# Optimization experiments

Measured on AMD Instinct MI355X. Metric: run time of the kernel, lower is better.

Reference implementation:

```python
import jax, jax.numpy as jnp
import numpy as np

B, S, F, H = 128, 1024, 512, 128


def setup_inputs() -> dict:
    key = jax.random.key(0)
    ks = jax.random.split(key, 12)
    # ragged valid lengths; force one full-length sequence so padded max == S
    lengths = jax.random.randint(ks[0], (B,), S // 4, S + 1)
    lengths = lengths.at[0].set(S)
    mask = (jnp.arange(S)[None, :] < lengths[:, None]).astype(jnp.float32)
    x = jax.random.normal(ks[1], (B, S, F), jnp.float32) * mask[:, :, None]
    s = 1.0 / np.sqrt(H)

    def u(k, shape):
        return jax.random.uniform(k, shape, jnp.float32, -s, s)

    return {
        "x": x,
        "Wp": u(ks[2], (H, F)), "bp": u(ks[3], (H,)),
        "Wih0": u(ks[4], (3 * H, H)), "Whh0": u(ks[5], (3 * H, H)),
        "bih0": u(ks[6], (3 * H,)), "bhh0": u(ks[7], (3 * H,)),
        "Wih1": u(ks[8], (3 * H, H)), "Whh1": u(ks[9], (3 * H, H)),
        "bih1": u(ks[10], (3 * H,)), "bhh1": u(ks[11], (3 * H,)),
    }


def _gru_layer(xs, Wih, Whh, bih, bhh):
    # xs: [S, B, H_in] -> outputs [S, B, H]; torch nn.GRU gate math (r,z,n order)
    xg = jnp.einsum('sbi,gi->sbg', xs, Wih) + bih  # precompute input gates [S,B,3H]
    Hh = Whh.shape[1]

    def step(h, xg_t):
        hg = h @ Whh.T + bhh
        xr, xz, xn = jnp.split(xg_t, 3, axis=-1)
        hr, hz, hn = jnp.split(hg, 3, axis=-1)
        r = jax.nn.sigmoid(xr + hr)
        z = jax.nn.sigmoid(xz + hz)
        n = jnp.tanh(xn + r * hn)
        h_new = (1.0 - z) * n + z * h
        return h_new, h_new

    h0 = jnp.zeros((xs.shape[1], Hh), xs.dtype)
    _, hs = jax.lax.scan(step, h0, xg)
    return hs


def reference(x, Wp, bp, Wih0, Whh0, bih0, bhh0, Wih1, Whh1, bih1, bhh1):
    # valid lengths: rows whose feature-sum is nonzero
    lengths = (jnp.sum(x, axis=-1) != 0).astype(jnp.int32).sum(axis=1)  # [B]
    proj = x @ Wp.T + bp  # [B,S,H]
    # sort by descending length (module returns outputs in SORTED order, no unsort)
    order = jnp.argsort(-lengths)
    sorted_lengths = lengths[order]
    xs = jnp.transpose(proj[order], (1, 0, 2))  # [S,B,H]
    h1 = _gru_layer(xs, Wih0, Whh0, bih0, bhh0)
    h2 = _gru_layer(h1, Wih1, Whh1, bih1, bhh1)
    out = jnp.transpose(h2, (1, 0, 2))  # [B,S,H]
    # pad_packed_sequence zeros outputs beyond each valid length
    valid = (jnp.arange(S)[None, :] < sorted_lengths[:, None]).astype(out.dtype)
    out = out * valid[:, :, None]
    # mean over padded length (max length == S here), zeros included, as in torch
    return out.mean(axis=1)
```

## Files before the change

kernel.cpp:

```cpp
#include <hip/hip_runtime.h>
#include <hip/hip_bf16.h>

#define BB 128
#define SS 1024
#define FF 512
#define HH 128
#define G3 384

typedef __attribute__((ext_vector_type(8))) short bf16x8;
typedef __attribute__((ext_vector_type(4))) float f32x4;
typedef _Float16 half2_t __attribute__((ext_vector_type(2)));

__global__ void zero_len_kernel(int* len) { len[threadIdx.x] = 0; }

__global__ void lengths_kernel(const float* __restrict__ x, int* __restrict__ len) {
    int wave = threadIdx.x >> 6;
    int lane = threadIdx.x & 63;
    long row = (long)blockIdx.x * 4 + wave;
    const float4* p = (const float4*)&x[row * FF + lane * 8];
    float4 v0 = p[0], v1 = p[1];
    float s = v0.x + v0.y + v0.z + v0.w + v1.x + v1.y + v1.z + v1.w;
    #pragma unroll
    for (int off = 32; off > 0; off >>= 1) s += __shfl_down(s, off, 64);
    if (lane == 0 && s != 0.0f) atomicAdd(&len[row >> 10], 1);
}

__global__ void rank_kernel(const int* __restrict__ len, int* __restrict__ rank) {
    int i = threadIdx.x;
    int li = len[i];
    int r = 0;
    for (int jj = 0; jj < BB; jj++) {
        int lj = len[jj];
        if (lj > li || (lj == li && jj < i)) r++;
    }
    rank[i] = r;
}

__device__ __forceinline__ short bf_hi(float w, float& hf) {
    unsigned u = __builtin_bit_cast(unsigned, w);
    unsigned r = (u + 0x7FFFu + ((u >> 16) & 1u)) & 0xFFFF0000u;
    hf = __builtin_bit_cast(float, r);
    return (short)(r >> 16);
}
__device__ __forceinline__ short bf_rn(float w) {
    unsigned u = __builtin_bit_cast(unsigned, w);
    unsigned r = u + 0x7FFFu + ((u >> 16) & 1u);
    return (short)(r >> 16);
}

__global__ __launch_bounds__(256) void gemm_mfma(
    const float* __restrict__ A, const float* __restrict__ W,
    const float* __restrict__ bias, float* __restrict__ C,
    int M, int N, int K)
{
    const int tid  = threadIdx.x;
    const int wvid = tid >> 6;
    const int lane = tid & 63;
    const int m0   = blockIdx.x * 64 + wvid * 16;
    const int n0   = blockIdx.y * 128;
    const int KS   = K >> 5;

    __shared__ __align__(16) short sh[2][8][64][8];

    f32x4 acc[8];
    #pragma unroll
    for (int i = 0; i < 8; i++) acc[i] = (f32x4){0.f, 0.f, 0.f, 0.f};

    const int arow = m0 + (lane & 15);
    const int koff = (lane >> 4) << 3;

    for (int ks = 0; ks < KS; ks++) {
        __syncthreads();
        #pragma unroll
        for (int i = 0; i < 2; i++) {
            int p  = tid + i * 256;
            int nt = p >> 6, ln = p & 63;
            const float* src = &W[(size_t)(n0 + nt * 16 + (ln & 15)) * K
                                  + ks * 32 + ((ln >> 4) << 3)];
            float w8[8];
            *(float4*)&w8[0] = *(const float4*)&src[0];
            *(float4*)&w8[4] = *(const float4*)&src[4];
            short hi8[8], lo8[8];
            #pragma unroll
            for (int e = 0; e < 8; e++) {
                float hf; hi8[e] = bf_hi(w8[e], hf);
                lo8[e] = bf_rn(w8[e] - hf);
            }
            *(bf16x8*)&sh[0][nt][ln][0] = *(bf16x8*)hi8;
            *(bf16x8*)&sh[1][nt][ln][0] = *(bf16x8*)lo8;
        }
        const float* ap = &A[(size_t)arow * K + ks * 32 + koff];
        float av[8];
        *(float4*)&av[0] = *(const float4*)&ap[0];
        *(float4*)&av[4] = *(const float4*)&ap[4];
        short ah[8], al[8];
        #pragma unroll
        for (int e = 0; e < 8; e++) {
            float hf; ah[e] = bf_hi(av[e], hf);
            al[e] = bf_rn(av[e] - hf);
        }
        bf16x8 ahi = *(bf16x8*)ah, alo = *(bf16x8*)al;
        __syncthreads();
        #pragma unroll
        for (int nt = 0; nt < 8; nt++) {
            bf16x8 bhi = *(bf16x8*)&sh[0][nt][lane][0];
            bf16x8 blo = *(bf16x8*)&sh[1][nt][lane][0];
            acc[nt] = __builtin_amdgcn_mfma_f32_16x16x32_bf16(ahi, bhi, acc[nt], 0, 0, 0);
            acc[nt] = __builtin_amdgcn_mfma_f32_16x16x32_bf16(ahi, blo, acc[nt], 0, 0, 0);
            acc[nt] = __builtin_amdgcn_mfma_f32_16x16x32_bf16(alo, bhi, acc[nt], 0, 0, 0);
        }
    }
    const int crow = m0 + ((lane >> 4) << 2);
    const int ccol = n0 + (lane & 15);
    #pragma unroll
    for (int nt = 0; nt < 8; nt++) {
        int col = ccol + nt * 16;
        float bv = bias[col];
        #pragma unroll
        for (int r = 0; r < 4; r++)
            C[(size_t)(crow + r) * N + col] = acc[nt][r] + bv;
    }
}

__device__ __forceinline__ float fast_sigmoid(float x) {
    return __builtin_amdgcn_rcpf(1.0f + __expf(-x));
}
__device__ __forceinline__ float fast_tanh(float x) {
    return 1.0f - 2.0f * __builtin_amdgcn_rcpf(1.0f + __expf(2.0f * x));
}
__device__ __forceinline__ half2_t bc16(unsigned u) {
    return __builtin_bit_cast(half2_t, u);
}
__device__ __forceinline__ unsigned pk16(float x, float y) {
    half2_t h; h[0] = (_Float16)x; h[1] = (_Float16)y;
    return __builtin_bit_cast(unsigned, h);
}
__device__ __forceinline__ float fdot2_(half2_t a, half2_t b, float c) {
#if __has_builtin(__builtin_amdgcn_fdot2)
    return __builtin_amdgcn_fdot2(a, b, c, false);
#else
    return c + (float)a[0] * (float)b[0] + (float)a[1] * (float)b[1];
#endif
}

template<int FINAL>
__global__ __launch_bounds__(1024, 4) void gru_rec(
    const float* __restrict__ xg,
    const float* __restrict__ Whh,
    const float* __restrict__ bhh,
    float* __restrict__ h_out,
    const int* __restrict__ len,
    const int* __restrict__ rank)
{
    const int b   = blockIdx.x;
    const int tid = threadIdx.x;
    const int j   = tid >> 3;
    const int k8  = tid & 7;

    __shared__ __align__(16) _Float16 h16[2][HH];
    __shared__ __align__(16) float    h32[2][HH];

    unsigned wv[24];
    #pragma unroll
    for (int g = 0; g < 3; g++) {
        const float* wr = &Whh[(size_t)(g * HH + j) * HH + k8 * 16];
        #pragma unroll
        for (int m = 0; m < 8; m++) wv[g * 8 + m] = pk16(wr[2 * m], wr[2 * m + 1]);
    }

    float b_r = 0.f, b_z = 0.f, b_n = 0.f;
    if (k8 == 0) { b_r = bhh[j]; b_z = bhh[HH + j]; b_n = bhh[2 * HH + j]; }
    const float* xgb = xg + (size_t)b * SS * G3;

    if (tid < HH) { h16[0][tid] = (_Float16)0.f; h32[0][tid] = 0.f; }
    float hprev = 0.0f, osum = 0.0f;
    const int L = FINAL ? len[b] : 0;

    float xr = 0.f, xz = 0.f, xn = 0.f;
    if (k8 == 0) { xr = xgb[j]; xz = xgb[HH + j]; xn = xgb[2 * HH + j]; }
    __syncthreads();

    for (int t = 0; t < SS; t++) {
        #pragma unroll
        for (int m = 0; m < 24; m += 4)
            asm volatile("" : "+v"(wv[m]), "+v"(wv[m + 1]),
                              "+v"(wv[m + 2]), "+v"(wv[m + 3]));

        if (!FINAL && t > 0 && tid >= 64 && tid < 96) {
            int c = tid - 64;
            float4 hv = ((const float4*)h32[t & 1])[c];
            *(float4*)&h_out[((size_t)b * SS + (t - 1)) * HH + c * 4] = hv;
        }
        float nxr = 0.f, nxz = 0.f, nxn = 0.f;
        if (k8 == 0 && t + 1 < SS) {
            const float* p = xgb + (size_t)(t + 1) * G3;
            nxr = p[j]; nxz = p[HH + j]; nxn = p[2 * HH + j];
        }
        const unsigned* hp = (const unsigned*)(&h16[t & 1][0]) + k8 * 8;
        uint4 hv0 = *(const uint4*)hp;
        uint4 hv1 = *(const uint4*)(hp + 4);
        half2_t q0 = bc16(hv0.x), q1 = bc16(hv0.y), q2 = bc16(hv0.z), q3 = bc16(hv0.w);
        half2_t q4 = bc16(hv1.x), q5 = bc16(hv1.y), q6 = bc16(hv1.z), q7 = bc16(hv1.w);

        float a0, a1, a2, c0, c1, c2;
        a0 = fdot2_(bc16(wv[0]),  q0, 0.f); c0 = fdot2_(bc16(wv[1]),  q1, 0.f);
        a0 = fdot2_(bc16(wv[2]),  q2, a0);  c0 = fdot2_(bc16(wv[3]),  q3, c0);
        a0 = fdot2_(bc16(wv[4]),  q4, a0);  c0 = fdot2_(bc16(wv[5]),  q5, c0);
        a0 = fdot2_(bc16(wv[6]),  q6, a0);  c0 = fdot2_(bc16(wv[7]),  q7, c0);
        a1 = fdot2_(bc16(wv[8]),  q0, 0.f); c1 = fdot2_(bc16(wv[9]),  q1, 0.f);
        a1 = fdot2_(bc16(wv[10]), q2, a1);  c1 = fdot2_(bc16(wv[11]), q3, c1);
        a1 = fdot2_(bc16(wv[12]), q4, a1);  c1 = fdot2_(bc16(wv[13]), q5, c1);
        a1 = fdot2_(bc16(wv[14]), q6, a1);  c1 = fdot2_(bc16(wv[15]), q7, c1);
        a2 = fdot2_(bc16(wv[16]), q0, 0.f); c2 = fdot2_(bc16(wv[17]), q1, 0.f);
        a2 = fdot2_(bc16(wv[18]), q2, a2);  c2 = fdot2_(bc16(wv[19]), q3, c2);
        a2 = fdot2_(bc16(wv[20]), q4, a2);  c2 = fdot2_(bc16(wv[21]), q5, c2);
        a2 = fdot2_(bc16(wv[22]), q6, a2);  c2 = fdot2_(bc16(wv[23]), q7, c2);

        float s0 = a0 + c0, s1 = a1 + c1, s2 = a2 + c2;
        s0 += __shfl_xor(s0, 1, 64); s1 += __shfl_xor(s1, 1, 64); s2 += __shfl_xor(s2, 1, 64);
        s0 += __shfl_xor(s0, 2, 64); s1 += __shfl_xor(s1, 2, 64); s2 += __shfl_xor(s2, 2, 64);
        s0 += __shfl_xor(s0, 4, 64); s1 += __shfl_xor(s1, 4, 64); s2 += __shfl_xor(s2, 4, 64);

        if (k8 == 0) {
            float r = fast_sigmoid(xr + s0 + b_r);
            float z = fast_sigmoid(xz + s1 + b_z);
            float n = fast_tanh(xn + r * (s2 + b_n));
            float h = (1.0f - z) * n + z * hprev;
            hprev = h;
            h16[(t + 1) & 1][j] = (_Float16)h;
            h32[(t + 1) & 1][j] = h;
            if (FINAL) { if (t < L) osum += h; }
        }
        xr = nxr; xz = nxz; xn = nxn;
        __syncthreads();
    }
    if (!FINAL && tid >= 64 && tid < 96) {
        int c = tid - 64;
        float4 hv = ((const float4*)h32[SS & 1])[c];
        *(float4*)&h_out[((size_t)b * SS + (SS - 1)) * HH + c * 4] = hv;
    }
    if (FINAL && k8 == 0) {
        h_out[(size_t)rank[b] * HH + j] = osum * (1.0f / (float)SS);
    }
}

extern "C" void kernel_launch(void* const* d_in, const int* in_sizes, int n_in,
                              void* d_out, int out_size, void* d_ws, size_t ws_size,
                              hipStream_t stream) {
    const float* x    = (const float*)d_in[0];
    const float* Wp   = (const float*)d_in[1];
    const float* bp   = (const float*)d_in[2];
    const float* Wih0 = (const float*)d_in[3];
    const float* Whh0 = (const float*)d_in[4];
    const float* bih0 = (const float*)d_in[5];
    const float* bhh0 = (const float*)d_in[6];
    const float* Wih1 = (const float*)d_in[7];
    const float* Whh1 = (const float*)d_in[8];
    const float* bih1 = (const float*)d_in[9];
    const float* bhh1 = (const float*)d_in[10];
    float* out = (float*)d_out;

    int* len  = (int*)d_ws;
    int* rank = len + 128;
    float* proj = (float*)((char*)d_ws + 4096);
    float* xgb  = proj + (size_t)BB * SS * HH;

    zero_len_kernel<<<1, 128, 0, stream>>>(len);
    lengths_kernel<<<(BB * SS) / 4, 256, 0, stream>>>(x, len);
    rank_kernel<<<1, 128, 0, stream>>>(len, rank);

    gemm_mfma<<<dim3(BB * SS / 64, 1), 256, 0, stream>>>(x, Wp, bp, proj,
                                                         BB * SS, HH, FF);
    gemm_mfma<<<dim3(BB * SS / 64, 3), 256, 0, stream>>>(proj, Wih0, bih0, xgb,
                                                         BB * SS, G3, HH);
    gru_rec<0><<<BB, 1024, 0, stream>>>(xgb, Whh0, bhh0, proj, len, rank);

    gemm_mfma<<<dim3(BB * SS / 64, 3), 256, 0, stream>>>(proj, Wih1, bih1, xgb,
                                                         BB * SS, G3, HH);
    gru_rec<1><<<BB, 1024, 0, stream>>>(xgb, Whh1, bhh1, out, len, rank);
}
```

Baseline: 2.451 ms.

## Stage packed fp16 Whh in LDS and halve GRU recurrence block size

A new pre-pass packs each recurrent weight matrix into an fp16 layout suited to how it is read. The GRU recurrence kernel copies that packed matrix into shared memory (96 KB) and runs with 512 threads instead of 1024, so each thread handles a quarter of a row instead of an eighth. This trades register-resident weights for LDS reads each step and saves one shuffle-reduction stage and half the wavefronts in the per-step barrier. The risk is added LDS bandwidth and latency on the serial critical path, plus the large shared allocation limiting occupancy.

```diff
diff --git a/kernel.cpp b/kernel.cpp
--- a/kernel.cpp
+++ b/kernel.cpp
@@ -143,10 +143,22 @@
 #endif
 }
 
+__global__ void pack_whh(const float* __restrict__ Whh, uint4* __restrict__ wp) {
+    int tid = threadIdx.x, r = blockIdx.x;
+    int g = r >> 2, i = r & 3, j = tid >> 2, kq = tid & 3;
+    const float* src = &Whh[(size_t)(g * HH + j) * HH + kq * 32 + i * 8];
+    uint4 o;
+    o.x = pk16(src[0], src[1]);
+    o.y = pk16(src[2], src[3]);
+    o.z = pk16(src[4], src[5]);
+    o.w = pk16(src[6], src[7]);
+    wp[r * 512 + tid] = o;
+}
+
 template<int FINAL>
-__global__ __launch_bounds__(1024, 4) void gru_rec(
+__global__ __launch_bounds__(512) void gru_rec(
+    const uint4* __restrict__ wp,
     const float* __restrict__ xg,
-    const float* __restrict__ Whh,
     const float* __restrict__ bhh,
     float* __restrict__ h_out,
     const int* __restrict__ len,
@@ -154,22 +166,18 @@
 {
     const int b   = blockIdx.x;
     const int tid = threadIdx.x;
-    const int j   = tid >> 3;
-    const int k8  = tid & 7;
-
+    const int j   = tid >> 2;
+    const int kq  = tid & 3;
+
+    __shared__ __align__(16) uint4    wlds[12 * 512];
     __shared__ __align__(16) _Float16 h16[2][HH];
     __shared__ __align__(16) float    h32[2][HH];
 
-    unsigned wv[24];
     #pragma unroll
-    for (int g = 0; g < 3; g++) {
-        const float* wr = &Whh[(size_t)(g * HH + j) * HH + k8 * 16];
-        #pragma unroll
-        for (int m = 0; m < 8; m++) wv[g * 8 + m] = pk16(wr[2 * m], wr[2 * m + 1]);
-    }
+    for (int r = 0; r < 12; r++) wlds[r * 512 + tid] = wp[r * 512 + tid];
 
     float b_r = 0.f, b_z = 0.f, b_n = 0.f;
-    if (k8 == 0) { b_r = bhh[j]; b_z = bhh[HH + j]; b_n = bhh[2 * HH + j]; }
+    if (kq == 0) { b_r = bhh[j]; b_z = bhh[HH + j]; b_n = bhh[2 * HH + j]; }
     const float* xgb = xg + (size_t)b * SS * G3;
 
     if (tid < HH) { h16[0][tid] = (_Float16)0.f; h32[0][tid] = 0.f; }
@@ -177,14 +185,14 @@
     const int L = FINAL ? len[b] : 0;
 
     float xr = 0.f, xz = 0.f, xn = 0.f;
-    if (k8 == 0) { xr = xgb[j]; xz = xgb[HH + j]; xn = xgb[2 * HH + j]; }
+    if (kq == 0) { xr = xgb[j]; xz = xgb[HH + j]; xn = xgb[2 * HH + j]; }
     __syncthreads();
 
     for (int t = 0; t < SS; t++) {
-        #pragma unroll
-        for (int m = 0; m < 24; m += 4)
-            asm volatile("" : "+v"(wv[m]), "+v"(wv[m + 1]),
-                              "+v"(wv[m + 2]), "+v"(wv[m + 3]));
+        int base = 0;
+        asm volatile("" : "+v"(base));
+        const uint4* wlA = wlds + tid + base;
+        const uint4* wlB = wlds + 8 * 512 + tid + base;
 
         if (!FINAL && t > 0 && tid >= 64 && tid < 96) {
             int c = tid - 64;
@@ -192,36 +200,58 @@
             *(float4*)&h_out[((size_t)b * SS + (t - 1)) * HH + c * 4] = hv;
         }
         float nxr = 0.f, nxz = 0.f, nxn = 0.f;
-        if (k8 == 0 && t + 1 < SS) {
+        if (kq == 0 && t + 1 < SS) {
             const float* p = xgb + (size_t)(t + 1) * G3;
             nxr = p[j]; nxz = p[HH + j]; nxn = p[2 * HH + j];
         }
-        const unsigned* hp = (const unsigned*)(&h16[t & 1][0]) + k8 * 8;
-        uint4 hv0 = *(const uint4*)hp;
-        uint4 hv1 = *(const uint4*)(hp + 4);
-        half2_t q0 = bc16(hv0.x), q1 = bc16(hv0.y), q2 = bc16(hv0.z), q3 = bc16(hv0.w);
-        half2_t q4 = bc16(hv1.x), q5 = bc16(hv1.y), q6 = bc16(hv1.z), q7 = bc16(hv1.w);
-
-        float a0, a1, a2, c0, c1, c2;
-        a0 = fdot2_(bc16(wv[0]),  q0, 0.f); c0 = fdot2_(bc16(wv[1]),  q1, 0.f);
-        a0 = fdot2_(bc16(wv[2]),  q2, a0);  c0 = fdot2_(bc16(wv[3]),  q3, c0);
-        a0 = fdot2_(bc16(wv[4]),  q4, a0);  c0 = fdot2_(bc16(wv[5]),  q5, c0);
-        a0 = fdot2_(bc16(wv[6]),  q6, a0);  c0 = fdot2_(bc16(wv[7]),  q7, c0);
-        a1 = fdot2_(bc16(wv[8]),  q0, 0.f); c1 = fdot2_(bc16(wv[9]),  q1, 0.f);
-        a1 = fdot2_(bc16(wv[10]), q2, a1);  c1 = fdot2_(bc16(wv[11]), q3, c1);
-        a1 = fdot2_(bc16(wv[12]), q4, a1);  c1 = fdot2_(bc16(wv[13]), q5, c1);
-        a1 = fdot2_(bc16(wv[14]), q6, a1);  c1 = fdot2_(bc16(wv[15]), q7, c1);
-        a2 = fdot2_(bc16(wv[16]), q0, 0.f); c2 = fdot2_(bc16(wv[17]), q1, 0.f);
-        a2 = fdot2_(bc16(wv[18]), q2, a2);  c2 = fdot2_(bc16(wv[19]), q3, c2);
-        a2 = fdot2_(bc16(wv[20]), q4, a2);  c2 = fdot2_(bc16(wv[21]), q5, c2);
-        a2 = fdot2_(bc16(wv[22]), q6, a2);  c2 = fdot2_(bc16(wv[23]), q7, c2);
-
-        float s0 = a0 + c0, s1 = a1 + c1, s2 = a2 + c2;
+        const uint4* hp = (const uint4*)(&h16[t & 1][0]) + kq * 4;
+        uint4 hq0 = hp[0], hq1 = hp[1], hq2 = hp[2], hq3 = hp[3];
+
+        float s0, s1, s2;
+        {
+            uint4 w0 = wlA[0 * 512], w1 = wlA[1 * 512], w2 = wlA[2 * 512], w3 = wlA[3 * 512];
+            float aA = fdot2_(bc16(w0.x), bc16(hq0.x), 0.f);
+            float aB = fdot2_(bc16(w0.y), bc16(hq0.y), 0.f);
+            aA = fdot2_(bc16(w0.z), bc16(hq0.z), aA); aB = fdot2_(bc16(w0.w), bc16(hq0.w), aB);
+            aA = fdot2_(bc16(w1.x), bc16(hq1.x), aA); aB = fdot2_(bc16(w1.y), bc16(hq1.y), aB);
+            aA = fdot2_(bc16(w1.z), bc16(hq1.z), aA); aB = fdot2_(bc16(w1.w), bc16(hq1.w), aB);
+            aA = fdot2_(bc16(w2.x), bc16(hq2.x), aA); aB = fdot2_(bc16(w2.y), bc16(hq2.y), aB);
+            aA = fdot2_(bc16(w2.z), bc16(hq2.z), aA); aB = fdot2_(bc16(w2.w), bc16(hq2.w), aB);
+            aA = fdot2_(bc16(w3.x), bc16(hq3.x), aA); aB = fdot2_(bc16(w3.y), bc16(hq3.y), aB);
+            aA = fdot2_(bc16(w3.z), bc16(hq3.z), aA); aB = fdot2_(bc16(w3.w), bc16(hq3.w), aB);
+            s0 = aA + aB;
+        }
+        {
+            uint4 w0 = wlA[4 * 512], w1 = wlA[5 * 512], w2 = wlA[6 * 512], w3 = wlA[7 * 512];
+            float aA = fdot2_(bc16(w0.x), bc16(hq0.x), 0.f);
+            float aB = fdot2_(bc16(w0.y), bc16(hq0.y), 0.f);
+            aA = fdot2_(bc16(w0.z), bc16(hq0.z), aA); aB = fdot2_(bc16(w0.w), bc16(hq0.w), aB);
+            aA = fdot2_(bc16(w1.x), bc16(hq1.x), aA); aB = fdot2_(bc16(w1.y), bc16(hq1.y), aB);
+            aA = fdot2_(bc16(w1.z), bc16(hq1.z), aA); aB = fdot2_(bc16(w1.w), bc16(hq1.w), aB);
+            aA = fdot2_(bc16(w2.x), bc16(hq2.x), aA); aB = fdot2_(bc16(w2.y), bc16(hq2.y), aB);
+            aA = fdot2_(bc16(w2.z), bc16(hq2.z), aA); aB = fdot2_(bc16(w2.w), bc16(hq2.w), aB);
+            aA = fdot2_(bc16(w3.x), bc16(hq3.x), aA); aB = fdot2_(bc16(w3.y), bc16(hq3.y), aB);
+            aA = fdot2_(bc16(w3.z), bc16(hq3.z), aA); aB = fdot2_(bc16(w3.w), bc16(hq3.w), aB);
+            s1 = aA + aB;
+        }
+        {
+            uint4 w0 = wlB[0 * 512], w1 = wlB[1 * 512], w2 = wlB[2 * 512], w3 = wlB[3 * 512];
+            float aA = fdot2_(bc16(w0.x), bc16(hq0.x), 0.f);
+            float aB = fdot2_(bc16(w0.y), bc16(hq0.y), 0.f);
+            aA = fdot2_(bc16(w0.z), bc16(hq0.z), aA); aB = fdot2_(bc16(w0.w), bc16(hq0.w), aB);
+            aA = fdot2_(bc16(w1.x), bc16(hq1.x), aA); aB = fdot2_(bc16(w1.y), bc16(hq1.y), aB);
+            aA = fdot2_(bc16(w1.z), bc16(hq1.z), aA); aB = fdot2_(bc16(w1.w), bc16(hq1.w), aB);
+            aA = fdot2_(bc16(w2.x), bc16(hq2.x), aA); aB = fdot2_(bc16(w2.y), bc16(hq2.y), aB);
+            aA = fdot2_(bc16(w2.z), bc16(hq2.z), aA); aB = fdot2_(bc16(w2.w), bc16(hq2.w), aB);
+            aA = fdot2_(bc16(w3.x), bc16(hq3.x), aA); aB = fdot2_(bc16(w3.y), bc16(hq3.y), aB);
+            aA = fdot2_(bc16(w3.z), bc16(hq3.z), aA); aB = fdot2_(bc16(w3.w), bc16(hq3.w), aB);
+            s2 = aA + aB;
+        }
+
         s0 += __shfl_xor(s0, 1, 64); s1 += __shfl_xor(s1, 1, 64); s2 += __shfl_xor(s2, 1, 64);
         s0 += __shfl_xor(s0, 2, 64); s1 += __shfl_xor(s1, 2, 64); s2 += __shfl_xor(s2, 2, 64);
-        s0 += __shfl_xor(s0, 4, 64); s1 += __shfl_xor(s1, 4, 64); s2 += __shfl_xor(s2, 4, 64);
-
-        if (k8 == 0) {
+
+        if (kq == 0) {
             float r = fast_sigmoid(xr + s0 + b_r);
             float z = fast_sigmoid(xz + s1 + b_z);
             float n = fast_tanh(xn + r * (s2 + b_n));
@@ -239,7 +269,7 @@
         float4 hv = ((const float4*)h32[SS & 1])[c];
         *(float4*)&h_out[((size_t)b * SS + (SS - 1)) * HH + c * 4] = hv;
     }
-    if (FINAL && k8 == 0) {
+    if (FINAL && kq == 0) {
         h_out[(size_t)rank[b] * HH + j] = osum * (1.0f / (float)SS);
     }
 }
@@ -262,20 +292,24 @@
 
     int* len  = (int*)d_ws;
     int* rank = len + 128;
-    float* proj = (float*)((char*)d_ws + 4096);
+    uint4* wp0 = (uint4*)((char*)d_ws + 4096);
+    uint4* wp1 = wp0 + 12 * 512;
+    float* proj = (float*)((char*)d_ws + 4096 + 2 * 12 * 512 * 16 + 4096);
     float* xgb  = proj + (size_t)BB * SS * HH;
 
     zero_len_kernel<<<1, 128, 0, stream>>>(len);
     lengths_kernel<<<(BB * SS) / 4, 256, 0, stream>>>(x, len);
     rank_kernel<<<1, 128, 0, stream>>>(len, rank);
+    pack_whh<<<12, 512, 0, stream>>>(Whh0, wp0);
+    pack_whh<<<12, 512, 0, stream>>>(Whh1, wp1);
 
     gemm_mfma<<<dim3(BB * SS / 64, 1), 256, 0, stream>>>(x, Wp, bp, proj,
                                                          BB * SS, HH, FF);
     gemm_mfma<<<dim3(BB * SS / 64, 3), 256, 0, stream>>>(proj, Wih0, bih0, xgb,
                                                          BB * SS, G3, HH);
-    gru_rec<0><<<BB, 1024, 0, stream>>>(xgb, Whh0, bhh0, proj, len, rank);
+    gru_rec<0><<<BB, 512, 0, stream>>>(wp0, xgb, bhh0, proj, len, rank);
 
     gemm_mfma<<<dim3(BB * SS / 64, 3), 256, 0, stream>>>(proj, Wih1, bih1, xgb,
                                                          BB * SS, G3, HH);
-    gru_rec<1><<<BB, 1024, 0, stream>>>(xgb, Whh1, bhh1, out, len, rank);
-}
+    gru_rec<1><<<BB, 512, 0, stream>>>(wp1, xgb, bhh1, out, len, rank);
+}
```

Result: faster. 2.162 ms (-11.8%).

## Shrink GRU recurrence to 256-thread blocks with Whh held in AGPRs

Applied to the files above, without the earlier changes.

The recurrent kernel drops from 1024 to 256 threads per block. Each thread now computes two hidden units over a 32-wide slice of K, and the 96 packed fp16 weight words per thread sit in accumulation registers (AGPRs), read back each step with v_accvgpr_read. The aim is a cheaper per-step __syncthreads, a shorter shuffle reduction (2 levels instead of 3), and vectorized float2 gate loads and stores. In exchange each thread does about four times more serial dot-product work per step, plus an AGPR read per weight word, which lengthens the per-timestep critical path.

```diff
diff --git a/kernel.cpp b/kernel.cpp
--- a/kernel.cpp
+++ b/kernel.cpp
@@ -143,8 +143,13 @@
 #endif
 }
 
+#define AW(N) asm volatile("v_accvgpr_write_b32 a" #N ", %0" :: "v"(wt[(N) & 15]) : "a" #N)
+#define DOT(N, ACC) do { unsigned _w; \
+    asm volatile("v_accvgpr_read_b32 %0, a" #N : "=v"(_w)); \
+    ACC = fdot2_(bc16(_w), bc16(hw[(N) & 15]), ACC); } while (0)
+
 template<int FINAL>
-__global__ __launch_bounds__(1024, 4) void gru_rec(
+__global__ __launch_bounds__(256, 1) void gru_rec(
     const float* __restrict__ xg,
     const float* __restrict__ Whh,
     const float* __restrict__ bhh,
@@ -154,84 +159,142 @@
 {
     const int b   = blockIdx.x;
     const int tid = threadIdx.x;
-    const int j   = tid >> 3;
-    const int k8  = tid & 7;
-
-    __shared__ __align__(16) _Float16 h16[2][HH];
+    const int j2  = tid >> 2;
+    const int kq  = tid & 3;
+    const int j0  = 2 * j2, j1 = 2 * j2 + 1;
+
+    __shared__ __align__(16) unsigned h16u[2][64];
     __shared__ __align__(16) float    h32[2][HH];
 
-    unsigned wv[24];
-    #pragma unroll
-    for (int g = 0; g < 3; g++) {
-        const float* wr = &Whh[(size_t)(g * HH + j) * HH + k8 * 16];
-        #pragma unroll
-        for (int m = 0; m < 8; m++) wv[g * 8 + m] = pk16(wr[2 * m], wr[2 * m + 1]);
-    }
-
-    float b_r = 0.f, b_z = 0.f, b_n = 0.f;
-    if (k8 == 0) { b_r = bhh[j]; b_z = bhh[HH + j]; b_n = bhh[2 * HH + j]; }
+    unsigned wt[16];
+    { const float* wr = &Whh[(size_t)(0 * HH + j0) * HH + kq * 32];
+      #pragma unroll
+      for (int m = 0; m < 16; m++) wt[m] = pk16(wr[2*m], wr[2*m+1]); }
+    AW(0);  AW(1);  AW(2);  AW(3);  AW(4);  AW(5);  AW(6);  AW(7);
+    AW(8);  AW(9);  AW(10); AW(11); AW(12); AW(13); AW(14); AW(15);
+    { const float* wr = &Whh[(size_t)(1 * HH + j0) * HH + kq * 32];
+      #pragma unroll
+      for (int m = 0; m < 16; m++) wt[m] = pk16(wr[2*m], wr[2*m+1]); }
+    AW(16); AW(17); AW(18); AW(19); AW(20); AW(21); AW(22); AW(23);
+    AW(24); AW(25); AW(26); AW(27); AW(28); AW(29); AW(30); AW(31);
+    { const float* wr = &Whh[(size_t)(2 * HH + j0) * HH + kq * 32];
+      #pragma unroll
+      for (int m = 0; m < 16; m++) wt[m] = pk16(wr[2*m], wr[2*m+1]); }
+    AW(32); AW(33); AW(34); AW(35); AW(36); AW(37); AW(38); AW(39);
+    AW(40); AW(41); AW(42); AW(43); AW(44); AW(45); AW(46); AW(47);
+    { const float* wr = &Whh[(size_t)(0 * HH + j1) * HH + kq * 32];
+      #pragma unroll
+      for (int m = 0; m < 16; m++) wt[m] = pk16(wr[2*m], wr[2*m+1]); }
+    AW(48); AW(49); AW(50); AW(51); AW(52); AW(53); AW(54); AW(55);
+    AW(56); AW(57); AW(58); AW(59); AW(60); AW(61); AW(62); AW(63);
+    { const float* wr = &Whh[(size_t)(1 * HH + j1) * HH + kq * 32];
+      #pragma unroll
+      for (int m = 0; m < 16; m++) wt[m] = pk16(wr[2*m], wr[2*m+1]); }
+    AW(64); AW(65); AW(66); AW(67); AW(68); AW(69); AW(70); AW(71);
+    AW(72); AW(73); AW(74); AW(75); AW(76); AW(77); AW(78); AW(79);
+    { const float* wr = &Whh[(size_t)(2 * HH + j1) * HH + kq * 32];
+      #pragma unroll
+      for (int m = 0; m < 16; m++) wt[m] = pk16(wr[2*m], wr[2*m+1]); }
+    AW(80); AW(81); AW(82); AW(83); AW(84); AW(85); AW(86); AW(87);
+    AW(88); AW(89); AW(90); AW(91); AW(92); AW(93); AW(94); AW(95);
+
+    float2 brv = {0.f, 0.f}, bzv = {0.f, 0.f}, bnv = {0.f, 0.f};
+    if (kq == 0) {
+        brv = *(const float2*)&bhh[j0];
+        bzv = *(const float2*)&bhh[HH + j0];
+        bnv = *(const float2*)&bhh[2 * HH + j0];
+    }
     const float* xgb = xg + (size_t)b * SS * G3;
 
-    if (tid < HH) { h16[0][tid] = (_Float16)0.f; h32[0][tid] = 0.f; }
-    float hprev = 0.0f, osum = 0.0f;
+    if (tid < 64)  { h16u[0][tid] = 0u; }
+    if (tid < 128) { h32[0][tid] = 0.f; }
+    float hprev0 = 0.f, hprev1 = 0.f, osum0 = 0.f, osum1 = 0.f;
     const int L = FINAL ? len[b] : 0;
 
-    float xr = 0.f, xz = 0.f, xn = 0.f;
-    if (k8 == 0) { xr = xgb[j]; xz = xgb[HH + j]; xn = xgb[2 * HH + j]; }
+    float2 xrv = {0,0}, xzv = {0,0}, xnv = {0,0};
+    if (kq == 0) {
+        xrv = *(const float2*)&xgb[j0];
+        xzv = *(const float2*)&xgb[HH + j0];
+        xnv = *(const float2*)&xgb[2 * HH + j0];
+    }
     __syncthreads();
 
     for (int t = 0; t < SS; t++) {
-        #pragma unroll
-        for (int m = 0; m < 24; m += 4)
-            asm volatile("" : "+v"(wv[m]), "+v"(wv[m + 1]),
-                              "+v"(wv[m + 2]), "+v"(wv[m + 3]));
+        const int cb = t & 1, nb = (t + 1) & 1;
 
         if (!FINAL && t > 0 && tid >= 64 && tid < 96) {
             int c = tid - 64;
-            float4 hv = ((const float4*)h32[t & 1])[c];
+            float4 hv = ((const float4*)h32[cb])[c];
             *(float4*)&h_out[((size_t)b * SS + (t - 1)) * HH + c * 4] = hv;
         }
-        float nxr = 0.f, nxz = 0.f, nxn = 0.f;
-        if (k8 == 0 && t + 1 < SS) {
+        float2 nxr = {0,0}, nxz = {0,0}, nxn = {0,0};
+        if (kq == 0 && t + 1 < SS) {
             const float* p = xgb + (size_t)(t + 1) * G3;
-            nxr = p[j]; nxz = p[HH + j]; nxn = p[2 * HH + j];
-        }
-        const unsigned* hp = (const unsigned*)(&h16[t & 1][0]) + k8 * 8;
-        uint4 hv0 = *(const uint4*)hp;
-        uint4 hv1 = *(const uint4*)(hp + 4);
-        half2_t q0 = bc16(hv0.x), q1 = bc16(hv0.y), q2 = bc16(hv0.z), q3 = bc16(hv0.w);
-        half2_t q4 = bc16(hv1.x), q5 = bc16(hv1.y), q6 = bc16(hv1.z), q7 = bc16(hv1.w);
-
-        float a0, a1, a2, c0, c1, c2;
-        a0 = fdot2_(bc16(wv[0]),  q0, 0.f); c0 = fdot2_(bc16(wv[1]),  q1, 0.f);
-        a0 = fdot2_(bc16(wv[2]),  q2, a0);  c0 = fdot2_(bc16(wv[3]),  q3, c0);
-        a0 = fdot2_(bc16(wv[4]),  q4, a0);  c0 = fdot2_(bc16(wv[5]),  q5, c0);
-        a0 = fdot2_(bc16(wv[6]),  q6, a0);  c0 = fdot2_(bc16(wv[7]),  q7, c0);
-        a1 = fdot2_(bc16(wv[8]),  q0, 0.f); c1 = fdot2_(bc16(wv[9]),  q1, 0.f);
-        a1 = fdot2_(bc16(wv[10]), q2, a1);  c1 = fdot2_(bc16(wv[11]), q3, c1);
-        a1 = fdot2_(bc16(wv[12]), q4, a1);  c1 = fdot2_(bc16(wv[13]), q5, c1);
-        a1 = fdot2_(bc16(wv[14]), q6, a1);  c1 = fdot2_(bc16(wv[15]), q7, c1);
-        a2 = fdot2_(bc16(wv[16]), q0, 0.f); c2 = fdot2_(bc16(wv[17]), q1, 0.f);
-        a2 = fdot2_(bc16(wv[18]), q2, a2);  c2 = fdot2_(bc16(wv[19]), q3, c2);
-        a2 = fdot2_(bc16(wv[20]), q4, a2);  c2 = fdot2_(bc16(wv[21]), q5, c2);
-        a2 = fdot2_(bc16(wv[22]), q6, a2);  c2 = fdot2_(bc16(wv[23]), q7, c2);
-
-        float s0 = a0 + c0, s1 = a1 + c1, s2 = a2 + c2;
-        s0 += __shfl_xor(s0, 1, 64); s1 += __shfl_xor(s1, 1, 64); s2 += __shfl_xor(s2, 1, 64);
-        s0 += __shfl_xor(s0, 2, 64); s1 += __shfl_xor(s1, 2, 64); s2 += __shfl_xor(s2, 2, 64);
-        s0 += __shfl_xor(s0, 4, 64); s1 += __shfl_xor(s1, 4, 64); s2 += __shfl_xor(s2, 4, 64);
-
-        if (k8 == 0) {
-            float r = fast_sigmoid(xr + s0 + b_r);
-            float z = fast_sigmoid(xz + s1 + b_z);
-            float n = fast_tanh(xn + r * (s2 + b_n));
-            float h = (1.0f - z) * n + z * hprev;
-            hprev = h;
-            h16[(t + 1) & 1][j] = (_Float16)h;
-            h32[(t + 1) & 1][j] = h;
-            if (FINAL) { if (t < L) osum += h; }
-        }
-        xr = nxr; xz = nxz; xn = nxn;
+            nxr = *(const float2*)&p[j0];
+            nxz = *(const float2*)&p[HH + j0];
+            nxn = *(const float2*)&p[2 * HH + j0];
+        }
+        const uint4* hp = (const uint4*)&h16u[cb][kq * 16];
+        uint4 q0 = hp[0], q1 = hp[1], q2 = hp[2], q3 = hp[3];
+        unsigned hw[16] = {q0.x,q0.y,q0.z,q0.w, q1.x,q1.y,q1.z,q1.w,
+                           q2.x,q2.y,q2.z,q2.w, q3.x,q3.y,q3.z,q3.w};
+
+        float rA, rB, zA, zB, nA, nB;
+        rA = 0.f; rB = 0.f;
+        DOT(0,rA);  DOT(1,rB);  DOT(2,rA);  DOT(3,rB);
+        DOT(4,rA);  DOT(5,rB);  DOT(6,rA);  DOT(7,rB);
+        DOT(8,rA);  DOT(9,rB);  DOT(10,rA); DOT(11,rB);
+        DOT(12,rA); DOT(13,rB); DOT(14,rA); DOT(15,rB);
+        zA = 0.f; zB = 0.f;
+        DOT(16,zA); DOT(17,zB); DOT(18,zA); DOT(19,zB);
+        DOT(20,zA); DOT(21,zB); DOT(22,zA); DOT(23,zB);
+        DOT(24,zA); DOT(25,zB); DOT(26,zA); DOT(27,zB);
+        DOT(28,zA); DOT(29,zB); DOT(30,zA); DOT(31,zB);
+        nA = 0.f; nB = 0.f;
+        DOT(32,nA); DOT(33,nB); DOT(34,nA); DOT(35,nB);
+        DOT(36,nA); DOT(37,nB); DOT(38,nA); DOT(39,nB);
+        DOT(40,nA); DOT(41,nB); DOT(42,nA); DOT(43,nB);
+        DOT(44,nA); DOT(45,nB); DOT(46,nA); DOT(47,nB);
+        float sr0 = rA + rB, sz0 = zA + zB, sn0 = nA + nB;
+        rA = 0.f; rB = 0.f;
+        DOT(48,rA); DOT(49,rB); DOT(50,rA); DOT(51,rB);
+        DOT(52,rA); DOT(53,rB); DOT(54,rA); DOT(55,rB);
+        DOT(56,rA); DOT(57,rB); DOT(58,rA); DOT(59,rB);
+        DOT(60,rA); DOT(61,rB); DOT(62,rA); DOT(63,rB);
+        zA = 0.f; zB = 0.f;
+        DOT(64,zA); DOT(65,zB); DOT(66,zA); DOT(67,zB);
+        DOT(68,zA); DOT(69,zB); DOT(70,zA); DOT(71,zB);
+        DOT(72,zA); DOT(73,zB); DOT(74,zA); DOT(75,zB);
+        DOT(76,zA); DOT(77,zB); DOT(78,zA); DOT(79,zB);
+        nA = 0.f; nB = 0.f;
+        DOT(80,nA); DOT(81,nB); DOT(82,nA); DOT(83,nB);
+        DOT(84,nA); DOT(85,nB); DOT(86,nA); DOT(87,nB);
+        DOT(88,nA); DOT(89,nB); DOT(90,nA); DOT(91,nB);
+        DOT(92,nA); DOT(93,nB); DOT(94,nA); DOT(95,nB);
+        float sr1 = rA + rB, sz1 = zA + zB, sn1 = nA + nB;
+
+        sr0 += __shfl_xor(sr0, 1, 64); sr0 += __shfl_xor(sr0, 2, 64);
+        sz0 += __shfl_xor(sz0, 1, 64); sz0 += __shfl_xor(sz0, 2, 64);
+        sn0 += __shfl_xor(sn0, 1, 64); sn0 += __shfl_xor(sn0, 2, 64);
+        sr1 += __shfl_xor(sr1, 1, 64); sr1 += __shfl_xor(sr1, 2, 64);
+        sz1 += __shfl_xor(sz1, 1, 64); sz1 += __shfl_xor(sz1, 2, 64);
+        sn1 += __shfl_xor(sn1, 1, 64); sn1 += __shfl_xor(sn1, 2, 64);
+
+        if (kq == 0) {
+            float r0 = fast_sigmoid(xrv.x + sr0 + brv.x);
+            float z0 = fast_sigmoid(xzv.x + sz0 + bzv.x);
+            float n0 = fast_tanh(xnv.x + r0 * (sn0 + bnv.x));
+            float h0 = (1.0f - z0) * n0 + z0 * hprev0;
+            float r1 = fast_sigmoid(xrv.y + sr1 + brv.y);
+            float z1 = fast_sigmoid(xzv.y + sz1 + bzv.y);
+            float n1 = fast_tanh(xnv.y + r1 * (sn1 + bnv.y));
+            float h1 = (1.0f - z1) * n1 + z1 * hprev1;
+            hprev0 = h0; hprev1 = h1;
+            h16u[nb][j2] = pk16(h0, h1);
+            *(float2*)&h32[nb][j0] = make_float2(h0, h1);
+            if (FINAL) { if (t < L) { osum0 += h0; osum1 += h1; } }
+        }
+        xrv = nxr; xzv = nxz; xnv = nxn;
         __syncthreads();
     }
     if (!FINAL && tid >= 64 && tid < 96) {
@@ -239,8 +302,9 @@
         float4 hv = ((const float4*)h32[SS & 1])[c];
         *(float4*)&h_out[((size_t)b * SS + (SS - 1)) * HH + c * 4] = hv;
     }
-    if (FINAL && k8 == 0) {
-        h_out[(size_t)rank[b] * HH + j] = osum * (1.0f / (float)SS);
+    if (FINAL && kq == 0) {
+        float2 o = make_float2(osum0 * (1.0f / (float)SS), osum1 * (1.0f / (float)SS));
+        *(float2*)&h_out[(size_t)rank[b] * HH + j0] = o;
     }
 }
 
@@ -273,9 +337,9 @@
                                                          BB * SS, HH, FF);
     gemm_mfma<<<dim3(BB * SS / 64, 3), 256, 0, stream>>>(proj, Wih0, bih0, xgb,
                                                          BB * SS, G3, HH);
-    gru_rec<0><<<BB, 1024, 0, stream>>>(xgb, Whh0, bhh0, proj, len, rank);
+    gru_rec<0><<<BB, 256, 0, stream>>>(xgb, Whh0, bhh0, proj, len, rank);
 
     gemm_mfma<<<dim3(BB * SS / 64, 3), 256, 0, stream>>>(proj, Wih1, bih1, xgb,
                                                          BB * SS, G3, HH);
-    gru_rec<1><<<BB, 1024, 0, stream>>>(xgb, Whh1, bhh1, out, len, rank);
-}
+    gru_rec<1><<<BB, 256, 0, stream>>>(xgb, Whh1, bhh1, out, len, rank);
+}
```

Result: slower. 2.707 ms (+10.4%).
